# Kernel optimization log

Hardware: AMD Instinct MI355X
Metric: run time of the kernel (lower is better)

Reference implementation:

```python
import jax, jax.numpy as jnp
import numpy as np

HIDDEN_NF = 256
ATOMICA_DIM = 512
NUM_HEADS = 4
HEAD_DIM = HIDDEN_NF // NUM_HEADS
EDGE_CUTOFF = 10.0
N_LIG = 1024
N_POCKET = 8192
BOX = 30.0  # Angstrom box so the cutoff mask is selective


def _lin(key, fan_in, fan_out):
    kw, kb = jax.random.split(key)
    s = 1.0 / np.sqrt(fan_in)
    W = jax.random.uniform(kw, (fan_in, fan_out), jnp.float32, -s, s)
    b = jax.random.uniform(kb, (fan_out,), jnp.float32, -s, s)
    return W, b


def setup_inputs() -> dict:
    key = jax.random.key(0)
    ks = jax.random.split(key, 12)
    h_lig = jax.random.normal(ks[0], (N_LIG, HIDDEN_NF), jnp.float32)
    x_lig = jax.random.uniform(ks[1], (N_LIG, 3), jnp.float32) * BOX
    h_atomica = jax.random.normal(ks[2], (N_POCKET, ATOMICA_DIM), jnp.float32)
    x_pocket = jax.random.uniform(ks[3], (N_POCKET, 3), jnp.float32) * BOX
    qw, qb = _lin(ks[4], HIDDEN_NF, HIDDEN_NF)
    kw, kb = _lin(ks[5], ATOMICA_DIM, HIDDEN_NF)
    vw, vb = _lin(ks[6], ATOMICA_DIM, HIDDEN_NF)
    ow, ob = _lin(ks[7], HIDDEN_NF, HIDDEN_NF)
    e1w, e1b = _lin(ks[8], 1, HIDDEN_NF)
    e2w, e2b = _lin(ks[9], HIDDEN_NF, NUM_HEADS)
    c1w, c1b = _lin(ks[10], HIDDEN_NF, HIDDEN_NF)
    c2w, c2b = _lin(ks[11], HIDDEN_NF, 1)
    return dict(h_lig=h_lig, x_lig=x_lig, h_atomica=h_atomica, x_pocket=x_pocket,
                qw=qw, qb=qb, kw=kw, kb=kb, vw=vw, vb=vb, ow=ow, ob=ob,
                e1w=e1w, e1b=e1b, e2w=e2w, e2b=e2b,
                c1w=c1w, c1b=c1b, c2w=c2w, c2b=c2b)


def reference(h_lig, x_lig, h_atomica, x_pocket,
              qw, qb, kw, kb, vw, vb, ow, ob,
              e1w, e1b, e2w, e2b, c1w, c1b, c2w, c2b):
    N_lig = h_lig.shape[0]
    silu = jax.nn.silu
    # pairwise geometry: [N_lig, N_pocket, 3]
    rel_pos = x_pocket[None, :, :] - x_lig[:, None, :]
    distances = jnp.linalg.norm(rel_pos, axis=-1, keepdims=True)  # [Nl,Np,1]
    # edge bias MLP: [Nl,Np,num_heads]
    edge_attr = silu(distances @ e1w + e1b) @ e2w + e2b
    mask = distances[..., 0] < EDGE_CUTOFF  # [Nl,Np]
    Q = (h_lig @ qw + qb).reshape(N_lig, NUM_HEADS, HEAD_DIM)
    K = (h_atomica @ kw + kb).reshape(-1, NUM_HEADS, HEAD_DIM)
    V = (h_atomica @ vw + vb).reshape(-1, NUM_HEADS, HEAD_DIM)
    scores = jnp.einsum('ihd,jhd->ijh', Q, K) / np.sqrt(HEAD_DIM).astype(np.float32)
    scores = scores + edge_attr
    scores = jnp.where(mask[..., None], scores, -jnp.inf)
    attn = jax.nn.softmax(scores, axis=1)
    attn = jnp.where(jnp.isnan(attn), 0.0, attn)  # nan_to_num for fully-masked rows
    h_attended = jnp.einsum('ijh,jhd->ihd', attn, V).reshape(N_lig, HIDDEN_NF)
    h_out = h_lig + h_attended @ ow + ob
    # equivariant coordinate update
    normalized_rel_pos = rel_pos / (distances + 1e-8)
    avg_attn = attn.mean(axis=-1, keepdims=True)  # [Nl,Np,1]
    coord_messages = (avg_attn * normalized_rel_pos).sum(axis=1)  # [Nl,3]
    coord_scale = silu(h_attended @ c1w + c1b) @ c2w + c2b  # [Nl,1]
    x_out = x_lig + coord_scale * coord_messages
    return h_out, x_out
```

## Files before the change

kernel.cpp:

```cpp
#include <hip/hip_runtime.h>
#include <hip/hip_bf16.h>


#define NLIG   1024
#define NPOCK  8192
#define HIDDEN 256
#define ADIM   512
#define NHEAD  4
#define HDIM   64
#define NTAB   1024
#define NSPLIT 16
#define CHUNK  (NPOCK / NSPLIT)
#define NT     (CHUNK / 32)
#define LOG2E  1.4426950408889634f
#define QK_SCALE (0.125f * LOG2E)

typedef float f32x16 __attribute__((ext_vector_type(16)));
typedef short short8 __attribute__((ext_vector_type(8)));

union U4S8 { uint4 u; short8 s; };

static __device__ __forceinline__ float exp2h(float x) {
  float r; asm("v_exp_f32 %0, %1" : "=v"(r) : "v"(x)); return r;
}
static __device__ __forceinline__ float rsqh(float x) {
  float r; asm("v_rsq_f32 %0, %1" : "=v"(r) : "v"(x)); return r;
}
static __device__ __forceinline__ unsigned cvtpk(float lo, float hi) {
  unsigned r;
  asm("v_cvt_pk_bf16_f32 %0, %1, %2" : "=v"(r) : "v"(lo), "v"(hi));
  return r;
}
static __device__ __forceinline__ unsigned short f2bf(float f) {
  union { __hip_bfloat16 h; unsigned short u; } c;
  c.h = __float2bfloat16(f);
  return c.u;
}
static __device__ __forceinline__ float bf2f(unsigned u16) {
  union { unsigned uu; float f; } c;
  c.uu = u16 << 16;
  return c.f;
}
static __device__ __forceinline__ short8 load_bf8(const unsigned short* p) {
  U4S8 t; t.u = *(const uint4*)p; return t.s;
}
static __device__ __forceinline__ f32x16 mfma32(short8 a, short8 b, f32x16 c) {
  return __builtin_amdgcn_mfma_f32_32x32x16_bf16(a, b, c, 0, 0, 0);
}
static __device__ __forceinline__ size_t t8(int r, int c, int Cdiv8) {
  return ((size_t)((r >> 5) * Cdiv8 + (c >> 3)) << 8) + ((r & 31) << 3) + (c & 7);
}

#define NCASTA 1024
#define NCASTL 64
#define NTRANS 448
__global__ __launch_bounds__(256)
void prep_kernel(const float* __restrict__ hA, const float* __restrict__ hl,
                 const float* __restrict__ qw, const float* __restrict__ kw,
                 const float* __restrict__ vw, const float* __restrict__ ow,
                 const float* __restrict__ c1w,
                 const float* __restrict__ e1w, const float* __restrict__ e1b,
                 const float* __restrict__ e2w, const float* __restrict__ e2b,
                 unsigned short* __restrict__ hAb, unsigned short* __restrict__ hlb,
                 unsigned short* __restrict__ qwT, unsigned short* __restrict__ kwT,
                 unsigned short* __restrict__ vwT, unsigned short* __restrict__ owT,
                 unsigned short* __restrict__ c1wT, float* __restrict__ tabG) {
  int bx = blockIdx.x;
  int tid = threadIdx.x;
  if (bx < NCASTA + NCASTL) {
    const float* src; unsigned short* dst; int stride, Cdiv8, R0, C0;
    if (bx < NCASTA) {
      src = hA; dst = hAb; stride = ADIM; Cdiv8 = 64;
      R0 = (bx >> 3) * 64; C0 = (bx & 7) * 64;
    } else {
      int b = bx - NCASTA;
      src = hl; dst = hlb; stride = HIDDEN; Cdiv8 = 32;
      R0 = (b >> 2) * 64; C0 = (b & 3) * 64;
    }
    __shared__ float tf[64][65];
    int r = tid >> 2;
#pragma unroll
    for (int pass = 0; pass < 4; ++pass) {
      int c4 = (tid & 3) + pass * 4;
      float4 v = ((const float4*)(src + (size_t)(R0 + r) * stride + C0))[c4];
      tf[r][c4 * 4 + 0] = v.x; tf[r][c4 * 4 + 1] = v.y;
      tf[r][c4 * 4 + 2] = v.z; tf[r][c4 * 4 + 3] = v.w;
    }
    __syncthreads();
    unsigned* dstu = (unsigned*)dst;
    size_t tbase = (size_t)(R0 >> 5) * Cdiv8 + (C0 >> 3);
#pragma unroll
    for (int k = 0; k < 8; ++k) {
      int u = k * 256 + tid;
      int tile = u >> 7, w2 = u & 127;
      int rb = tile >> 3, cb = tile & 7;
      int rr = rb * 32 + (w2 >> 2);
      int c = cb * 8 + (w2 & 3) * 2;
      unsigned val = cvtpk(tf[rr][c], tf[rr][c + 1]);
      dstu[(tbase + (size_t)rb * Cdiv8 + cb) * 128 + w2] = val;
    }
  } else if (bx < NCASTA + NCASTL + NTRANS) {
    int b = bx - (NCASTA + NCASTL);
    const float* src; unsigned short* dst; int K;
    if (b < 64)       { src = qw;  dst = qwT;  K = 256; }
    else if (b < 192) { src = kw;  dst = kwT;  K = 512; b -= 64; }
    else if (b < 320) { src = vw;  dst = vwT;  K = 512; b -= 192; }
    else if (b < 384) { src = ow;  dst = owT;  K = 256; b -= 320; }
    else              { src = c1w; dst = c1wT; K = 256; b -= 384; }
    int kt = K / 32;
    int k0 = (b % kt) * 32, n0 = (b / kt) * 32;
    __shared__ float tile[32][33];
    int tx = tid & 31, ty = tid >> 5;
#pragma unroll
    for (int r = 0; r < 4; ++r)
      tile[ty + 8 * r][tx] = src[(k0 + ty + 8 * r) * 256 + n0 + tx];
    __syncthreads();
#pragma unroll
    for (int r = 0; r < 4; ++r)
      dst[t8(n0 + ty + 8 * r, k0 + tx, K >> 3)] = f2bf(tile[tx][ty + 8 * r]);
  } else {
    int eb = bx - (NCASTA + NCASTL + NTRANS);
    int w = tid >> 6, l = tid & 63;
    int entry = eb * 4 + w;
    float d = (entry + 0.5f) * (10.0f / NTAB);
    float a0 = 0.f, a1 = 0.f, a2 = 0.f, a3 = 0.f;
#pragma unroll
    for (int jj = 0; jj < 4; ++jj) {
      int j = l + jj * 64;
      float v = fmaf(d, e1w[j], e1b[j]);
      float s = v / (1.0f + __expf(-v));
      float4 w2 = ((const float4*)e2w)[j];
      a0 = fmaf(s, w2.x, a0);
      a1 = fmaf(s, w2.y, a1);
      a2 = fmaf(s, w2.z, a2);
      a3 = fmaf(s, w2.w, a3);
    }
#pragma unroll
    for (int m = 32; m >= 1; m >>= 1) {
      a0 += __shfl_xor(a0, m); a1 += __shfl_xor(a1, m);
      a2 += __shfl_xor(a2, m); a3 += __shfl_xor(a3, m);
    }
    if (l == 0) {
      tabG[0 * NTAB + entry] = (a0 + e2b[0]) * LOG2E;
      tabG[1 * NTAB + entry] = (a1 + e2b[1]) * LOG2E;
      tabG[2 * NTAB + entry] = (a2 + e2b[2]) * LOG2E;
      tabG[3 * NTAB + entry] = (a3 + e2b[3]) * LOG2E;
    }
  }
}

__global__ __launch_bounds__(256)
void proj_kernel(const unsigned short* __restrict__ hAb, const unsigned short* __restrict__ hlb,
                 const unsigned short* __restrict__ kwT, const unsigned short* __restrict__ vwT,
                 const unsigned short* __restrict__ qwT,
                 const float* __restrict__ kb, const float* __restrict__ vb,
                 const float* __restrict__ qb,
                 unsigned short* __restrict__ Kb, unsigned short* __restrict__ VTb,
                 unsigned short* __restrict__ Qb) {
  int tid = threadIdx.x;
  int w = tid >> 6, lane = tid & 63;
  int lo = lane & 31, hi = lane >> 5;
  int n0 = blockIdx.y * 64;
  if (blockIdx.x < 64) {
    int m0 = blockIdx.x * 128 + w * 32;
    const unsigned short* ap   = hAb + t8(m0 + lo, hi * 8, 64);
    const unsigned short* bk0p = kwT + t8(n0 + lo, hi * 8, 64);
    const unsigned short* bk1p = bk0p + 64 * 256;
    const unsigned short* bv0p = vwT + t8(n0 + lo, hi * 8, 64);
    const unsigned short* bv1p = bv0p + 64 * 256;
    f32x16 aK0, aK1, aV0, aV1;
#pragma unroll
    for (int i = 0; i < 16; ++i) { aK0[i] = 0.f; aK1[i] = 0.f; aV0[i] = 0.f; aV1[i] = 0.f; }
#pragma unroll 4
    for (int kk = 0; kk < ADIM / 16; ++kk) {
      short8 a   = load_bf8(ap + kk * 512);
      short8 bk0 = load_bf8(bk0p + kk * 512);
      short8 bk1 = load_bf8(bk1p + kk * 512);
      short8 bv0 = load_bf8(bv0p + kk * 512);
      short8 bv1 = load_bf8(bv1p + kk * 512);
      aK0 = mfma32(a, bk0, aK0);
      aK1 = mfma32(a, bk1, aK1);
      aV0 = mfma32(bv0, a, aV0);
      aV1 = mfma32(bv1, a, aV1);
    }
    float bnK0 = kb[n0 + lo], bnK1 = kb[n0 + 32 + lo];
#pragma unroll
    for (int g = 0; g < 4; ++g) {
#pragma unroll
      for (int rr = 0; rr < 4; ++rr) {
        int r = g * 4 + rr;
        int row = g * 8 + hi * 4 + rr;
        Kb[t8(m0 + row, n0 + lo, 32)]      = f2bf(aK0[r] + bnK0);
        Kb[t8(m0 + row, n0 + 32 + lo, 32)] = f2bf(aK1[r] + bnK1);
        VTb[t8(n0 + row, m0 + lo, 1024)]      = f2bf(aV0[r] + vb[n0 + row]);
        VTb[t8(n0 + 32 + row, m0 + lo, 1024)] = f2bf(aV1[r] + vb[n0 + 32 + row]);
      }
    }
  } else {
    int m0 = (blockIdx.x - 64) * 128 + w * 32;
    const unsigned short* ap  = hlb + t8(m0 + lo, hi * 8, 32);
    const unsigned short* b0p = qwT + t8(n0 + lo, hi * 8, 32);
    const unsigned short* b1p = b0p + 32 * 256;
    f32x16 a0, a1;
#pragma unroll
    for (int i = 0; i < 16; ++i) { a0[i] = 0.f; a1[i] = 0.f; }
#pragma unroll 8
    for (int kk = 0; kk < HIDDEN / 16; ++kk) {
      short8 a  = load_bf8(ap + kk * 512);
      short8 b0 = load_bf8(b0p + kk * 512);
      short8 b1 = load_bf8(b1p + kk * 512);
      a0 = mfma32(a, b0, a0);
      a1 = mfma32(a, b1, a1);
    }
    float bn0 = qb[n0 + lo], bn1 = qb[n0 + 32 + lo];
#pragma unroll
    for (int g = 0; g < 4; ++g) {
#pragma unroll
      for (int rr = 0; rr < 4; ++rr) {
        int r = g * 4 + rr;
        int m = m0 + g * 8 + hi * 4 + rr;
        Qb[t8(m, n0 + lo, 32)]      = f2bf(a0[r] + bn0);
        Qb[t8(m, n0 + 32 + lo, 32)] = f2bf(a1[r] + bn1);
      }
    }
  }
}

__global__ __launch_bounds__(256)
void attn_kernel(const unsigned short* __restrict__ Qbf, const unsigned short* __restrict__ Kbf,
                 const unsigned short* __restrict__ VTbf,
                 const float* __restrict__ x_lig, const float* __restrict__ x_pocket,
                 const float* __restrict__ tabG,
                 unsigned* __restrict__ partOb, float4* __restrict__ partZC) {
  __shared__ float4 xch[CHUNK];
  __shared__ float tab[NHEAD][NTAB];

  int tid = threadIdx.x;
  int h = tid >> 6;
  int lane = tid & 63;
  int lo = lane & 31, hi = lane >> 5;
  int qt = blockIdx.x & 31;
  int split = blockIdx.x >> 5;
  int q0 = qt * 32;
  int j0g = split * CHUNK;

  for (int i = tid; i < CHUNK; i += 256) {
    float x = x_pocket[(j0g + i) * 3 + 0];
    float y = x_pocket[(j0g + i) * 3 + 1];
    float z = x_pocket[(j0g + i) * 3 + 2];
    float4 v; v.x = x; v.y = y; v.z = z; v.w = 0.f;
    xch[i] = v;
  }
  for (int i = tid; i < NHEAD * NTAB; i += 256) ((float*)tab)[i] = tabG[i];
  __syncthreads();

  int q = q0 + lo;
  float xl0 = x_lig[q * 3 + 0];
  float xl1 = x_lig[q * 3 + 1];
  float xl2 = x_lig[q * 3 + 2];

  short8 qfr[4];
#pragma unroll
  for (int kk = 0; kk < 4; ++kk)
    qfr[kk] = load_bf8(Qbf + t8(q, h * HDIM + kk * 16 + hi * 8, 32));

  const unsigned short* kbp = Kbf + t8(j0g + lo, h * HDIM + hi * 8, 32);
  const unsigned short* vbp = VTbf + t8(h * HDIM + lo, j0g + hi * 8, 1024);

  f32x16 O0, O1;
#pragma unroll
  for (int i = 0; i < 16; ++i) { O0[i] = 0.f; O1[i] = 0.f; }
  float Z = 0.f, c0 = 0.f, c1 = 0.f, c2 = 0.f;

  short8 kcur[4];
#pragma unroll
  for (int kk = 0; kk < 4; ++kk) kcur[kk] = load_bf8(kbp + kk * 512);

#pragma unroll 1
  for (int t = 0; t < NT; ++t) {
    int jb = t * 32;
    int tn = (t + 1 < NT) ? (t + 1) : t;
    short8 knx0 = load_bf8(kbp + (size_t)tn * 8192 + 0 * 512);
    short8 knx1 = load_bf8(kbp + (size_t)tn * 8192 + 1 * 512);
    short8 knx2 = load_bf8(kbp + (size_t)tn * 8192 + 2 * 512);
    short8 knx3 = load_bf8(kbp + (size_t)tn * 8192 + 3 * 512);
    short8 v00 = load_bf8(vbp + (size_t)t * 1024);
    short8 v01 = load_bf8(vbp + (size_t)t * 1024 + 262144);
    short8 v10 = load_bf8(vbp + (size_t)t * 1024 + 512);
    short8 v11 = load_bf8(vbp + (size_t)t * 1024 + 512 + 262144);

    f32x16 s;
#pragma unroll
    for (int i = 0; i < 16; ++i) s[i] = 0.f;
    s = mfma32(kcur[0], qfr[0], s);
    s = mfma32(kcur[1], qfr[1], s);
    s = mfma32(kcur[2], qfr[2], s);
    s = mfma32(kcur[3], qfr[3], s);

    unsigned wp[8];
    float pprev = 0.f;
#pragma unroll
    for (int r = 0; r < 16; ++r) {
      int jl = (r & 3) + 8 * (r >> 2) + 4 * hi;
      float4 xp = xch[jb + jl];
      float dx = xp.x - xl0, dy = xp.y - xl1, dz = xp.z - xl2;
      float r2 = fmaf(dx, dx, fmaf(dy, dy, dz * dz));
      float r2c = fmaxf(r2, 1e-24f);
      float rinv = rsqh(r2c);
      float d = r2c * rinv;
      int idx = (int)(d * (NTAB / 10.0f));
      idx = idx > (NTAB - 1) ? (NTAB - 1) : idx;
      float b = tab[h][idx];
      float s2 = fmaf(s[r], QK_SCALE, b);
      float pe = (r2 < 100.0f) ? exp2h(s2) : 0.0f;
      Z += pe;
      float pr = pe * rinv;
      c0 = fmaf(pr, dx, c0);
      c1 = fmaf(pr, dy, c1);
      c2 = fmaf(pr, dz, c2);
      if (r & 1) wp[r >> 1] = cvtpk(pprev, pe); else pprev = pe;
    }
    {
      unsigned W0 = wp[0], W1 = wp[1], W2 = wp[2], W3 = wp[3];
      unsigned e01 = (unsigned)__shfl_xor((int)(hi ? W0 : W2), 32);
      unsigned e23 = (unsigned)__shfl_xor((int)(hi ? W1 : W3), 32);
      U4S8 pb;
      pb.u.x = hi ? e01 : W0;
      pb.u.y = hi ? e23 : W1;
      pb.u.z = hi ? W2 : e01;
      pb.u.w = hi ? W3 : e23;
      O0 = mfma32(v00, pb.s, O0);
      O1 = mfma32(v01, pb.s, O1);
    }
    {
      unsigned W0 = wp[4], W1 = wp[5], W2 = wp[6], W3 = wp[7];
      unsigned e01 = (unsigned)__shfl_xor((int)(hi ? W0 : W2), 32);
      unsigned e23 = (unsigned)__shfl_xor((int)(hi ? W1 : W3), 32);
      U4S8 pb;
      pb.u.x = hi ? e01 : W0;
      pb.u.y = hi ? e23 : W1;
      pb.u.z = hi ? W2 : e01;
      pb.u.w = hi ? W3 : e23;
      O0 = mfma32(v10, pb.s, O0);
      O1 = mfma32(v11, pb.s, O1);
    }
    kcur[0] = knx0; kcur[1] = knx1; kcur[2] = knx2; kcur[3] = knx3;
  }

  unsigned* po = partOb + ((size_t)(split * NLIG + q) * (HIDDEN / 2)) + h * (HDIM / 2);
#pragma unroll
  for (int g = 0; g < 4; ++g) {
    uint2 u0;
    u0.x = cvtpk(O0[g * 4 + 0], O0[g * 4 + 1]);
    u0.y = cvtpk(O0[g * 4 + 2], O0[g * 4 + 3]);
    *(uint2*)(po + g * 4 + hi * 2) = u0;
    uint2 u1;
    u1.x = cvtpk(O1[g * 4 + 0], O1[g * 4 + 1]);
    u1.y = cvtpk(O1[g * 4 + 2], O1[g * 4 + 3]);
    *(uint2*)(po + 16 + g * 4 + hi * 2) = u1;
  }
  float Zt = Z + __shfl_xor(Z, 32);
  float c0t = c0 + __shfl_xor(c0, 32);
  float c1t = c1 + __shfl_xor(c1, 32);
  float c2t = c2 + __shfl_xor(c2, 32);
  if (hi == 0) {
    float4 zc; zc.x = Zt; zc.y = c0t; zc.z = c1t; zc.w = c2t;
    partZC[(size_t)(split * NLIG + q) * NHEAD + h] = zc;
  }
}

__global__ __launch_bounds__(512)
void tail_kernel(const unsigned* __restrict__ partOb, const float4* __restrict__ partZC,
                 const unsigned short* __restrict__ owT, const unsigned short* __restrict__ c1wT,
                 const float* __restrict__ ob, const float* __restrict__ c1b,
                 const float* __restrict__ c2w, const float* __restrict__ c2b,
                 const float* __restrict__ h_lig, const float* __restrict__ x_lig,
                 float* __restrict__ hout, float* __restrict__ xout) {
  __shared__ unsigned hattL[32 * 128];
  __shared__ float invL[32][4];
  __shared__ float cmsgL[32][3];
  __shared__ float cscL[32];

  int t = threadIdx.x;
  int q0 = blockIdx.x * 32;

  if (t < 128) {
    int i = t >> 2, h = t & 3;
    float zz = 0.f, a0 = 0.f, a1 = 0.f, a2 = 0.f;
#pragma unroll
    for (int s = 0; s < NSPLIT; ++s) {
      float4 v = partZC[(size_t)(s * NLIG + q0 + i) * NHEAD + h];
      zz += v.x; a0 += v.y; a1 += v.z; a2 += v.w;
    }
    invL[i][h] = (zz > 0.f) ? 1.0f / zz : 0.f;
    float iv = (zz > 0.f) ? 0.25f / zz : 0.f;
    a0 *= iv; a1 *= iv; a2 *= iv;
    a0 += __shfl_xor(a0, 1); a0 += __shfl_xor(a0, 2);
    a1 += __shfl_xor(a1, 1); a1 += __shfl_xor(a1, 2);
    a2 += __shfl_xor(a2, 1); a2 += __shfl_xor(a2, 2);
    if (h == 0) { cmsgL[i][0] = a0; cmsgL[i][1] = a1; cmsgL[i][2] = a2; }
  }
  if (t < 32) cscL[t] = 0.f;
  __syncthreads();

  {
    int c2i = t & 127;
    int c = c2i * 2;
#pragma unroll
    for (int i = t >> 7; i < 32; i += 4) {
      float o0 = 0.f, o1 = 0.f;
#pragma unroll
      for (int s = 0; s < NSPLIT; ++s) {
        unsigned u = partOb[(size_t)(s * NLIG + q0 + i) * 128 + c2i];
        o0 += bf2f(u & 0xffffu);
        o1 += bf2f(u >> 16);
      }
      float inv = invL[i][c >> 6];
      hattL[(c >> 3) * 128 + i * 4 + ((c & 7) >> 1)] = cvtpk(o0 * inv, o1 * inv);
    }
  }
  __syncthreads();

  int w = t >> 6, lane = t & 63;
  int lo = lane & 31, hi = lane >> 5;
  int n = w * 32 + lo;
  const unsigned short* bo = owT + t8(n, hi * 8, 32);
  const unsigned short* bc = c1wT + t8(n, hi * 8, 32);
  f32x16 aO, aC;
#pragma unroll
  for (int i = 0; i < 16; ++i) { aO[i] = 0.f; aC[i] = 0.f; }
#pragma unroll 8
  for (int kk = 0; kk < 16; ++kk) {
    U4S8 av; av.u = *(const uint4*)&hattL[(kk * 2 + hi) * 128 + lo * 4];
    short8 b1 = load_bf8(bo + kk * 512);
    short8 b2 = load_bf8(bc + kk * 512);
    aO = mfma32(av.s, b1, aO);
    aC = mfma32(av.s, b2, aC);
  }
  float obn = ob[n], c1bn = c1b[n], c2wn = c2w[n];
#pragma unroll
  for (int g = 0; g < 4; ++g) {
#pragma unroll
    for (int rr = 0; rr < 4; ++rr) {
      int r = g * 4 + rr;
      int mi = g * 8 + hi * 4 + rr;
      int m = q0 + mi;
      hout[(size_t)m * HIDDEN + n] = aO[r] + obn + h_lig[(size_t)m * HIDDEN + n];
      float v = aC[r] + c1bn;
      float sg = v / (1.0f + exp2h(-LOG2E * v));
      float part = sg * c2wn;
#pragma unroll
      for (int msk = 16; msk >= 1; msk >>= 1) part += __shfl_xor(part, msk);
      if (lo == 0) atomicAdd(&cscL[mi], part);
    }
  }
  __syncthreads();

  if (t < 96) {
    int i = t / 3, d = t % 3;
    int q = q0 + i;
    xout[q * 3 + d] = x_lig[q * 3 + d] + (cscL[i] + c2b[0]) * cmsgL[i][d];
  }
}

extern "C" void kernel_launch(void* const* d_in, const int* in_sizes, int n_in,
                              void* d_out, int out_size, void* d_ws, size_t ws_size,
                              hipStream_t stream) {
  const float* h_lig  = (const float*)d_in[0];
  const float* x_lig  = (const float*)d_in[1];
  const float* h_atom = (const float*)d_in[2];
  const float* x_pock = (const float*)d_in[3];
  const float* qw  = (const float*)d_in[4];
  const float* qb  = (const float*)d_in[5];
  const float* kw  = (const float*)d_in[6];
  const float* kb  = (const float*)d_in[7];
  const float* vw  = (const float*)d_in[8];
  const float* vb  = (const float*)d_in[9];
  const float* ow  = (const float*)d_in[10];
  const float* ob  = (const float*)d_in[11];
  const float* e1w = (const float*)d_in[12];
  const float* e1b = (const float*)d_in[13];
  const float* e2w = (const float*)d_in[14];
  const float* e2b = (const float*)d_in[15];
  const float* c1w = (const float*)d_in[16];
  const float* c1b = (const float*)d_in[17];
  const float* c2w = (const float*)d_in[18];
  const float* c2b = (const float*)d_in[19];

  char* w = (char*)d_ws;
  unsigned short* hAb  = (unsigned short*)w; w += (size_t)NPOCK * ADIM * 2;
  unsigned short* hlb  = (unsigned short*)w; w += (size_t)NLIG * HIDDEN * 2;
  unsigned short* qwT  = (unsigned short*)w; w += 256 * 256 * 2;
  unsigned short* kwT  = (unsigned short*)w; w += 256 * 512 * 2;
  unsigned short* vwT  = (unsigned short*)w; w += 256 * 512 * 2;
  unsigned short* owT  = (unsigned short*)w; w += 256 * 256 * 2;
  unsigned short* c1wT = (unsigned short*)w; w += 256 * 256 * 2;
  unsigned short* Qb   = (unsigned short*)w; w += (size_t)NLIG * HIDDEN * 2;
  unsigned short* Kb   = (unsigned short*)w; w += (size_t)NPOCK * HIDDEN * 2;
  unsigned short* VTb  = (unsigned short*)w; w += (size_t)HIDDEN * NPOCK * 2;
  float* tabG          = (float*)w;          w += NHEAD * NTAB * 4;
  unsigned* partOb     = (unsigned*)w;       w += (size_t)NSPLIT * NLIG * HIDDEN * 2;
  float* partZC        = (float*)w;          w += (size_t)NSPLIT * NLIG * NHEAD * 4 * 4;

  float* hout = (float*)d_out;
  float* xout = ((float*)d_out) + (size_t)NLIG * HIDDEN;

  prep_kernel<<<NCASTA + NCASTL + NTRANS + NTAB / 4, 256, 0, stream>>>(
      h_atom, h_lig, qw, kw, vw, ow, c1w, e1w, e1b, e2w, e2b,
      hAb, hlb, qwT, kwT, vwT, owT, c1wT, tabG);
  proj_kernel<<<dim3(72, 4), 256, 0, stream>>>(
      hAb, hlb, kwT, vwT, qwT, kb, vb, qb, Kb, VTb, Qb);
  attn_kernel<<<32 * NSPLIT, 256, 0, stream>>>(Qb, Kb, VTb, x_lig, x_pock, tabG,
                                               partOb, (float4*)partZC);
  tail_kernel<<<32, 512, 0, stream>>>(partOb, (const float4*)partZC, owT, c1wT,
                                      ob, c1b, c2w, c2b, h_lig, x_lig, hout, xout);
}
```

Before: 183.4 us.

## Split attention key chunk across two wave groups per block and combine via LDS

Doubles the attention block to 512 threads: each head now has two waves that take alternating 32-key tiles of the chunk, and their partial O/Z/coord sums are merged through shared memory before being written out. This halves each wave's serial loop length and adds waves per CU to hide latency. The explicit K prefetch of the next tile is dropped. The second wave group's partial O is rounded to bf16 before the merge, so there is slight extra rounding error. There is also added LDS traffic and a block-wide sync.

```diff
diff --git a/kernel.cpp b/kernel.cpp
--- a/kernel.cpp
+++ b/kernel.cpp
@@ -11,7 +11,6 @@
 #define NTAB   1024
 #define NSPLIT 16
 #define CHUNK  (NPOCK / NSPLIT)
-#define NT     (CHUNK / 32)
 #define LOG2E  1.4426950408889634f
 #define QK_SCALE (0.125f * LOG2E)
 
@@ -226,7 +225,7 @@
   }
 }
 
-__global__ __launch_bounds__(256)
+__global__ __launch_bounds__(512, 4)
 void attn_kernel(const unsigned short* __restrict__ Qbf, const unsigned short* __restrict__ Kbf,
                  const unsigned short* __restrict__ VTbf,
                  const float* __restrict__ x_lig, const float* __restrict__ x_pocket,
@@ -234,9 +233,12 @@
                  unsigned* __restrict__ partOb, float4* __restrict__ partZC) {
   __shared__ float4 xch[CHUNK];
   __shared__ float tab[NHEAD][NTAB];
+  __shared__ unsigned Ocomb[NHEAD][32][32];
+  __shared__ float Zc[NHEAD][4][32];
 
   int tid = threadIdx.x;
-  int h = tid >> 6;
+  int wid = tid >> 6;
+  int h = wid & 3, sj = wid >> 2;
   int lane = tid & 63;
   int lo = lane & 31, hi = lane >> 5;
   int qt = blockIdx.x & 31;
@@ -244,14 +246,14 @@
   int q0 = qt * 32;
   int j0g = split * CHUNK;
 
-  for (int i = tid; i < CHUNK; i += 256) {
+  for (int i = tid; i < CHUNK; i += 512) {
     float x = x_pocket[(j0g + i) * 3 + 0];
     float y = x_pocket[(j0g + i) * 3 + 1];
     float z = x_pocket[(j0g + i) * 3 + 2];
     float4 v; v.x = x; v.y = y; v.z = z; v.w = 0.f;
     xch[i] = v;
   }
-  for (int i = tid; i < NHEAD * NTAB; i += 256) ((float*)tab)[i] = tabG[i];
+  for (int i = tid; i < NHEAD * NTAB; i += 512) ((float*)tab)[i] = tabG[i];
   __syncthreads();
 
   int q = q0 + lo;
@@ -264,38 +266,33 @@
   for (int kk = 0; kk < 4; ++kk)
     qfr[kk] = load_bf8(Qbf + t8(q, h * HDIM + kk * 16 + hi * 8, 32));
 
-  const unsigned short* kbp = Kbf + t8(j0g + lo, h * HDIM + hi * 8, 32);
-  const unsigned short* vbp = VTbf + t8(h * HDIM + lo, j0g + hi * 8, 1024);
+  const unsigned short* kbp = Kbf + t8(j0g + sj * 32 + lo, h * HDIM + hi * 8, 32);
+  const unsigned short* vbp = VTbf + t8(h * HDIM + lo, j0g + sj * 32 + hi * 8, 1024);
 
   f32x16 O0, O1;
 #pragma unroll
   for (int i = 0; i < 16; ++i) { O0[i] = 0.f; O1[i] = 0.f; }
   float Z = 0.f, c0 = 0.f, c1 = 0.f, c2 = 0.f;
 
-  short8 kcur[4];
-#pragma unroll
-  for (int kk = 0; kk < 4; ++kk) kcur[kk] = load_bf8(kbp + kk * 512);
-
 #pragma unroll 1
-  for (int t = 0; t < NT; ++t) {
-    int jb = t * 32;
-    int tn = (t + 1 < NT) ? (t + 1) : t;
-    short8 knx0 = load_bf8(kbp + (size_t)tn * 8192 + 0 * 512);
-    short8 knx1 = load_bf8(kbp + (size_t)tn * 8192 + 1 * 512);
-    short8 knx2 = load_bf8(kbp + (size_t)tn * 8192 + 2 * 512);
-    short8 knx3 = load_bf8(kbp + (size_t)tn * 8192 + 3 * 512);
-    short8 v00 = load_bf8(vbp + (size_t)t * 1024);
-    short8 v01 = load_bf8(vbp + (size_t)t * 1024 + 262144);
-    short8 v10 = load_bf8(vbp + (size_t)t * 1024 + 512);
-    short8 v11 = load_bf8(vbp + (size_t)t * 1024 + 512 + 262144);
+  for (int t = 0; t < CHUNK / 64; ++t) {
+    int jb = t * 64 + sj * 32;
+    short8 k0 = load_bf8(kbp + (size_t)t * 16384 + 0 * 512);
+    short8 k1 = load_bf8(kbp + (size_t)t * 16384 + 1 * 512);
+    short8 k2 = load_bf8(kbp + (size_t)t * 16384 + 2 * 512);
+    short8 k3 = load_bf8(kbp + (size_t)t * 16384 + 3 * 512);
+    short8 v00 = load_bf8(vbp + (size_t)t * 2048);
+    short8 v01 = load_bf8(vbp + (size_t)t * 2048 + 262144);
+    short8 v10 = load_bf8(vbp + (size_t)t * 2048 + 512);
+    short8 v11 = load_bf8(vbp + (size_t)t * 2048 + 512 + 262144);
 
     f32x16 s;
 #pragma unroll
     for (int i = 0; i < 16; ++i) s[i] = 0.f;
-    s = mfma32(kcur[0], qfr[0], s);
-    s = mfma32(kcur[1], qfr[1], s);
-    s = mfma32(kcur[2], qfr[2], s);
-    s = mfma32(kcur[3], qfr[3], s);
+    s = mfma32(k0, qfr[0], s);
+    s = mfma32(k1, qfr[1], s);
+    s = mfma32(k2, qfr[2], s);
+    s = mfma32(k3, qfr[3], s);
 
     unsigned wp[8];
     float pprev = 0.f;
@@ -344,28 +341,60 @@
       O0 = mfma32(v10, pb.s, O0);
       O1 = mfma32(v11, pb.s, O1);
     }
-    kcur[0] = knx0; kcur[1] = knx1; kcur[2] = knx2; kcur[3] = knx3;
-  }
-
-  unsigned* po = partOb + ((size_t)(split * NLIG + q) * (HIDDEN / 2)) + h * (HDIM / 2);
-#pragma unroll
-  for (int g = 0; g < 4; ++g) {
-    uint2 u0;
-    u0.x = cvtpk(O0[g * 4 + 0], O0[g * 4 + 1]);
-    u0.y = cvtpk(O0[g * 4 + 2], O0[g * 4 + 3]);
-    *(uint2*)(po + g * 4 + hi * 2) = u0;
-    uint2 u1;
-    u1.x = cvtpk(O1[g * 4 + 0], O1[g * 4 + 1]);
-    u1.y = cvtpk(O1[g * 4 + 2], O1[g * 4 + 3]);
-    *(uint2*)(po + 16 + g * 4 + hi * 2) = u1;
-  }
-  float Zt = Z + __shfl_xor(Z, 32);
-  float c0t = c0 + __shfl_xor(c0, 32);
-  float c1t = c1 + __shfl_xor(c1, 32);
-  float c2t = c2 + __shfl_xor(c2, 32);
-  if (hi == 0) {
-    float4 zc; zc.x = Zt; zc.y = c0t; zc.z = c1t; zc.w = c2t;
-    partZC[(size_t)(split * NLIG + q) * NHEAD + h] = zc;
+  }
+
+  if (sj == 1) {
+#pragma unroll
+    for (int g = 0; g < 4; ++g) {
+      int dp = g * 4 + hi * 2;
+      Ocomb[h][dp][lo]      = cvtpk(O0[g * 4 + 0], O0[g * 4 + 1]);
+      Ocomb[h][dp + 1][lo]  = cvtpk(O0[g * 4 + 2], O0[g * 4 + 3]);
+      Ocomb[h][dp + 16][lo] = cvtpk(O1[g * 4 + 0], O1[g * 4 + 1]);
+      Ocomb[h][dp + 17][lo] = cvtpk(O1[g * 4 + 2], O1[g * 4 + 3]);
+    }
+    float Zt = Z + __shfl_xor(Z, 32);
+    float c0t = c0 + __shfl_xor(c0, 32);
+    float c1t = c1 + __shfl_xor(c1, 32);
+    float c2t = c2 + __shfl_xor(c2, 32);
+    if (hi == 0) {
+      Zc[h][0][lo] = Zt; Zc[h][1][lo] = c0t; Zc[h][2][lo] = c1t; Zc[h][3][lo] = c2t;
+    }
+  }
+  __syncthreads();
+  if (sj == 0) {
+#pragma unroll
+    for (int g = 0; g < 4; ++g) {
+      int dp = g * 4 + hi * 2;
+      unsigned u;
+      u = Ocomb[h][dp][lo];      O0[g*4+0] += bf2f(u & 0xffffu); O0[g*4+1] += bf2f(u >> 16);
+      u = Ocomb[h][dp + 1][lo];  O0[g*4+2] += bf2f(u & 0xffffu); O0[g*4+3] += bf2f(u >> 16);
+      u = Ocomb[h][dp + 16][lo]; O1[g*4+0] += bf2f(u & 0xffffu); O1[g*4+1] += bf2f(u >> 16);
+      u = Ocomb[h][dp + 17][lo]; O1[g*4+2] += bf2f(u & 0xffffu); O1[g*4+3] += bf2f(u >> 16);
+    }
+    unsigned* po = partOb + ((size_t)(split * NLIG + q) * (HIDDEN / 2)) + h * (HDIM / 2);
+#pragma unroll
+    for (int g = 0; g < 4; ++g) {
+      uint2 u0;
+      u0.x = cvtpk(O0[g * 4 + 0], O0[g * 4 + 1]);
+      u0.y = cvtpk(O0[g * 4 + 2], O0[g * 4 + 3]);
+      *(uint2*)(po + g * 4 + hi * 2) = u0;
+      uint2 u1;
+      u1.x = cvtpk(O1[g * 4 + 0], O1[g * 4 + 1]);
+      u1.y = cvtpk(O1[g * 4 + 2], O1[g * 4 + 3]);
+      *(uint2*)(po + 16 + g * 4 + hi * 2) = u1;
+    }
+    float Zt = Z + __shfl_xor(Z, 32);
+    float c0t = c0 + __shfl_xor(c0, 32);
+    float c1t = c1 + __shfl_xor(c1, 32);
+    float c2t = c2 + __shfl_xor(c2, 32);
+    if (hi == 0) {
+      float4 zc;
+      zc.x = Zt + Zc[h][0][lo];
+      zc.y = c0t + Zc[h][1][lo];
+      zc.z = c1t + Zc[h][2][lo];
+      zc.w = c2t + Zc[h][3][lo];
+      partZC[(size_t)(split * NLIG + q) * NHEAD + h] = zc;
+    }
   }
 }
 
@@ -510,7 +539,7 @@
       hAb, hlb, qwT, kwT, vwT, owT, c1wT, tabG);
   proj_kernel<<<dim3(72, 4), 256, 0, stream>>>(
       hAb, hlb, kwT, vwT, qwT, kb, vb, qb, Kb, VTb, Qb);
-  attn_kernel<<<32 * NSPLIT, 256, 0, stream>>>(Qb, Kb, VTb, x_lig, x_pock, tabG,
+  attn_kernel<<<32 * NSPLIT, 512, 0, stream>>>(Qb, Kb, VTb, x_lig, x_pock, tabG,
                                                partOb, (float4*)partZC);
   tail_kernel<<<32, 512, 0, stream>>>(partOb, (const float4*)partZC, owT, c1wT,
                                       ob, c1b, c2w, c2b, h_lig, x_lig, hout, xout);
```

New measurement: 261.7 us. 1.43x slower.
